# Kernel tuning notes

Hardware: AMD Instinct MI355X
Metric: run time of the kernel (lower is better)

## Reference

```python
import jax, jax.numpy as jnp
import numpy as np

H = 2048          # hidden_size
NH = 16           # num_attention_heads
NKV = 4           # num_key_value_heads
HD = 128          # head_dim
B, S = 2, 2048
EPS = 1e-6


def _rms_norm(x, w):
    # RMSNorm over last dim (head_dim)
    var = jnp.mean(jnp.square(x), axis=-1, keepdims=True)
    return x * jax.lax.rsqrt(var + EPS) * w


def _rotate_half(x):
    x1, x2 = jnp.split(x, 2, axis=-1)
    return jnp.concatenate([-x2, x1], axis=-1)


def _apply_rope(x, cos, sin):
    # x: [b, s, h, d]; cos/sin: [s, d]
    c = cos[None, :, None, :]
    s = sin[None, :, None, :]
    return x * c + _rotate_half(x) * s


def setup_inputs() -> dict:
    key = jax.random.key(0)
    ks = jax.random.split(key, 12)
    hidden_states = jax.random.normal(ks[0], (B, S, H), dtype=jnp.float32)
    # RoPE tables (base 10000, full head_dim)
    inv_freq = 1.0 / (10000.0 ** (np.arange(0, HD, 2, dtype=np.float32) / HD))
    t = np.arange(S, dtype=np.float32)
    freqs = np.outer(t, inv_freq)                      # [S, HD/2]
    emb = np.concatenate([freqs, freqs], axis=-1)      # [S, HD]
    cos = jnp.asarray(np.cos(emb), dtype=jnp.float32)
    sin = jnp.asarray(np.sin(emb), dtype=jnp.float32)
    scale = 0.02
    Wq = jax.random.normal(ks[1], (H, NH * HD), jnp.float32) * scale
    bq = jax.random.normal(ks[2], (NH * HD,), jnp.float32) * scale
    Wk = jax.random.normal(ks[3], (H, NKV * HD), jnp.float32) * scale
    bk = jax.random.normal(ks[4], (NKV * HD,), jnp.float32) * scale
    Wv = jax.random.normal(ks[5], (H, NKV * HD), jnp.float32) * scale
    bv = jax.random.normal(ks[6], (NKV * HD,), jnp.float32) * scale
    Wo = jax.random.normal(ks[7], (NH * HD, H), jnp.float32) * scale
    bo = jax.random.normal(ks[8], (H,), jnp.float32) * scale
    q_norm_w = jnp.ones((HD,), jnp.float32)
    k_norm_w = jnp.ones((HD,), jnp.float32)
    cu_seqlens = jnp.array([0, S, 2 * S], dtype=jnp.int32)
    max_s = S
    return {"hidden_states": hidden_states, "cos": cos, "sin": sin,
            "Wq": Wq, "bq": bq, "Wk": Wk, "bk": bk, "Wv": Wv, "bv": bv,
            "Wo": Wo, "bo": bo, "q_norm_w": q_norm_w, "k_norm_w": k_norm_w,
            "cu_seqlens": cu_seqlens, "max_s": max_s}


def reference(hidden_states, cos, sin, Wq, bq, Wk, bk, Wv, bv, Wo, bo,
              q_norm_w, k_norm_w, cu_seqlens, max_s):
    b, s, _ = hidden_states.shape
    q = (hidden_states @ Wq + bq).reshape(b, s, NH, HD)
    k = (hidden_states @ Wk + bk).reshape(b, s, NKV, HD)
    v = (hidden_states @ Wv + bv).reshape(b, s, NKV, HD)
    q = _rms_norm(q, q_norm_w)
    k = _rms_norm(k, k_norm_w)
    q = _apply_rope(q, cos, sin)
    k = _apply_rope(k, cos, sin)
    # GQA: repeat_interleave kv heads to match query heads
    n_rep = NH // NKV
    k = jnp.repeat(k, n_rep, axis=2)   # [b, s, NH, HD]
    v = jnp.repeat(v, n_rep, axis=2)
    scale = 1.0 / jnp.sqrt(jnp.float32(HD))
    # scores: [b, h, s_q, s_k]
    scores = jnp.einsum('bqhd,bkhd->bhqk', q, k) * scale
    neg = jnp.finfo(scores.dtype).min
    causal = jnp.triu(jnp.ones((s, s), dtype=bool), k=1)
    scores = scores + jnp.where(causal, neg, 0.0)[None, None]
    weights = jax.nn.softmax(scores, axis=-1)
    attn = jnp.einsum('bhqk,bkhd->bqhd', weights, v).reshape(b, s, NH * HD)
    return attn @ Wo + bo
```

## Files before the change

### kernel.cpp

```cpp
#include <hip/hip_runtime.h>
#include <math.h>

#define H 2048
#define NH 16
#define NKV 4
#define HD 128
#define BB 2
#define SS 2048
#define NT (BB*SS)
#define NQK (NH*HD)
#define NKVD (NKV*HD)
#define NQKV (NQK + 2*NKVD)
#define EPSV 1e-6f
#define SM_SCALE 0.08838834764831845f

using s8v = __attribute__((ext_vector_type(8))) short;
using s4v = __attribute__((ext_vector_type(4))) short;
using f4v = __attribute__((ext_vector_type(4))) float;

typedef unsigned int __attribute__((address_space(1))) u32_g;
typedef unsigned int __attribute__((address_space(3))) u32_l;

__device__ inline float bf2f(short s){ unsigned u = ((unsigned)(unsigned short)s) << 16; return __builtin_bit_cast(float, u); }
__device__ inline short f2bf(float f){ unsigned u = __builtin_bit_cast(unsigned, f); u += 0x7FFF + ((u>>16)&1); return (short)(u>>16); }

__device__ inline f4v mfma16(s8v a, s8v b, f4v c){
    return __builtin_amdgcn_mfma_f32_16x16x32_bf16(a, b, c, 0, 0, 0);
}

__device__ inline void gl_lds16(const short* g, short* l){
    __builtin_amdgcn_global_load_lds((const u32_g*)g, (u32_l*)l, 16, 0, 0);
}


__global__ void cvt_f32_bf16(const float* __restrict__ in, short* __restrict__ out, int n4){
    int i = blockIdx.x*blockDim.x + threadIdx.x;
    int stride = gridDim.x*blockDim.x;
    for (; i < n4; i += stride){
        float4 v = reinterpret_cast<const float4*>(in)[i];
        s4v o = { f2bf(v.x), f2bf(v.y), f2bf(v.z), f2bf(v.w) };
        reinterpret_cast<s4v*>(out)[i] = o;
    }
}

__global__ __launch_bounds__(256) void transpose_cvt(const float* __restrict__ src, short* __restrict__ dst,
                                                     int R, int C){
    __shared__ short t[64][72];
    const int tid = threadIdx.x;
    const int r0 = blockIdx.y*64, c0 = blockIdx.x*64;
    #pragma unroll
    for (int it = 0; it < 4; ++it){
        int ch = tid + it*256;
        int row = ch >> 4, c4 = (ch & 15) * 4;
        float4 v = *reinterpret_cast<const float4*>(src + (size_t)(r0+row)*C + c0 + c4);
        t[row][c4+0] = f2bf(v.x); t[row][c4+1] = f2bf(v.y);
        t[row][c4+2] = f2bf(v.z); t[row][c4+3] = f2bf(v.w);
    }
    __syncthreads();
    #pragma unroll
    for (int it = 0; it < 4; ++it){
        int ch = tid + it*256;
        int cc = ch >> 4, r4 = (ch & 15) * 4;
        s4v o = { t[r4+0][cc], t[r4+1][cc], t[r4+2][cc], t[r4+3][cc] };
        *reinterpret_cast<s4v*>(dst + (size_t)(c0+cc)*R + r0 + r4) = o;
    }
}

__global__ void concat_b(const float* __restrict__ bq, const float* __restrict__ bk,
                         const float* __restrict__ bv, float* __restrict__ Bc){
    int i = blockIdx.x*blockDim.x + threadIdx.x;
    if (i < NQKV)
        Bc[i] = (i < NQK) ? bq[i] : (i < NQK+NKVD ? bk[i-NQK] : bv[i-NQK-NKVD]);
}


template<int OUT_F32>
__global__ __launch_bounds__(256) void gemm_bt(const short* __restrict__ A, const short* __restrict__ BT,
                                               const float* __restrict__ bias, void* __restrict__ Cout,
                                               int M, int N, int K){
    __shared__ short As[2][4096];
    __shared__ short Bs[2][4096];
    const int tid  = threadIdx.x;
    const int lane = tid & 63;
    const int wv   = tid >> 6;
    const int f    = lane & 15;
    const int g    = lane >> 4;
    const int m0   = blockIdx.y * 128;
    const int n0   = blockIdx.x * 128;
    const int mb   = (wv & 1) * 64;
    const int nb   = (wv >> 1) * 64;
    f4v acc[4][4] = {};

    const short* Abase = A  + (size_t)m0*K;
    const short* Bbase = BT + (size_t)n0*K;
    const int srow = (lane >> 2);
    const int scol = (lane & 3) * 8;

    auto STAGE = [&](int buf, int k0){
        #pragma unroll
        for (int c = 0; c < 2; ++c){
            int issue = wv + c*4;
            int row = issue*16 + srow;
            gl_lds16(Abase + (size_t)row*K + k0 + scol, &As[buf][issue*512]);
            gl_lds16(Bbase + (size_t)row*K + k0 + scol, &Bs[buf][issue*512]);
        }
    };

    STAGE(0, 0);
    asm volatile("s_waitcnt vmcnt(0)" ::: "memory");
    __syncthreads();
    int cur = 0;
    for (int k0 = 0; k0 < K; k0 += 32){
        if (k0 + 32 < K) STAGE(cur^1, k0 + 32);
        s8v a[4], bfr[4];
        #pragma unroll
        for (int i = 0; i < 4; ++i) a[i]   = *reinterpret_cast<const s8v*>(&As[cur][(mb + i*16 + f)*32 + g*8]);
        #pragma unroll
        for (int j = 0; j < 4; ++j) bfr[j] = *reinterpret_cast<const s8v*>(&Bs[cur][(nb + j*16 + f)*32 + g*8]);
        #pragma unroll
        for (int i = 0; i < 4; ++i)
            #pragma unroll
            for (int j = 0; j < 4; ++j)
                acc[i][j] = mfma16(a[i], bfr[j], acc[i][j]);
        asm volatile("s_waitcnt vmcnt(0)" ::: "memory");
        __syncthreads();
        cur ^= 1;
    }

    #pragma unroll
    for (int i = 0; i < 4; ++i){
        #pragma unroll
        for (int j = 0; j < 4; ++j){
            int col = n0 + nb + j*16 + f;
            float bvv = bias ? bias[col] : 0.f;
            #pragma unroll
            for (int r = 0; r < 4; ++r){
                int row = m0 + mb + i*16 + g*4 + r;
                float vv = acc[i][j][r] + bvv;
                if (OUT_F32) reinterpret_cast<float*>(Cout)[(size_t)row*N + col] = vv;
                else         reinterpret_cast<short*>(Cout)[(size_t)row*N + col] = f2bf(vv);
            }
        }
    }
}


__global__ __launch_bounds__(256) void norm_rope(short* __restrict__ qkv, const float* __restrict__ cosb,
                                                 const float* __restrict__ sinb, const float* __restrict__ qw,
                                                 const float* __restrict__ kw){
    int row  = blockIdx.x * 4 + (threadIdx.x >> 6);
    int lane = threadIdx.x & 63;
    const int QROWS = NT * NH;
    short* ptr; const float* w; float outscale; int token;
    if (row < QROWS){
        token = row >> 4; int h = row & 15;
        ptr = qkv + (size_t)token*NQKV + h*HD; w = qw; outscale = SM_SCALE;
    } else {
        int rr = row - QROWS;
        token = rr >> 2; int h = rr & 3;
        ptr = qkv + (size_t)token*NQKV + NQK + h*HD; w = kw; outscale = 1.f;
    }
    int s = token & (SS-1);
    float x1 = bf2f(ptr[lane]), x2 = bf2f(ptr[lane+64]);
    float ssq = x1*x1 + x2*x2;
    #pragma unroll
    for (int off = 32; off; off >>= 1) ssq += __shfl_xor(ssq, off, 64);
    float inv = rsqrtf(ssq * (1.f/128.f) + EPSV);
    float n1 = x1 * inv * w[lane];
    float n2 = x2 * inv * w[lane+64];
    float c1 = cosb[s*HD + lane], c2 = cosb[s*HD + lane + 64];
    float s1 = sinb[s*HD + lane], s2 = sinb[s*HD + lane + 64];
    float o1 = (n1*c1 - n2*s1) * outscale;
    float o2 = (n2*c2 + n1*s2) * outscale;
    ptr[lane]    = f2bf(o1);
    ptr[lane+64] = f2bf(o2);
}


__global__ __launch_bounds__(256) void vtrans(const short* __restrict__ qkv, short* __restrict__ Vt){
    __shared__ short t[64][72];
    const int tid = threadIdx.x;
    const int s0 = blockIdx.x*64, c0 = blockIdx.y*64, b = blockIdx.z;
    #pragma unroll
    for (int it = 0; it < 2; ++it){
        int ch = tid + it*256;
        int row = ch >> 3, col = (ch & 7)*8;
        s8v v = *reinterpret_cast<const s8v*>(qkv + (size_t)(b*SS + s0 + row)*NQKV + NQK + NKVD + c0 + col);
        *reinterpret_cast<s8v*>(&t[row][col]) = v;
    }
    __syncthreads();
    #pragma unroll
    for (int it = 0; it < 2; ++it){
        int ch = tid + it*256;
        int cc = ch >> 3, sc = (ch & 7)*8;
        s8v o;
        #pragma unroll
        for (int j = 0; j < 8; ++j) o[j] = t[sc + j][cc];
        *reinterpret_cast<s8v*>(Vt + (size_t)(b*NKVD + c0 + cc)*SS + s0 + sc) = o;
    }
}


__global__ __launch_bounds__(512, 4) void attn_fwd(const short* __restrict__ qkv, const short* __restrict__ Vt,
                                                   short* __restrict__ attn){
    __shared__ short Ks[2][8192];
    __shared__ short Vs[2][8192];
    __shared__ short Ps[8][1024];
    const int tid  = threadIdx.x;
    const int lane = tid & 63;
    const int w    = tid >> 6;
    const int f    = lane & 15;
    const int g    = lane >> 4;
    const int qt   = 63 - (int)blockIdx.x;
    const int kvh  = blockIdx.y;
    const int b    = blockIdx.z;
    const int h    = kvh*4 + (w >> 1);
    const int half = w & 1;
    const int q0   = qt * 32;
    const int qrow0 = q0 + half*16;
    char* Pb = (char*)Ps[w];

    auto STAGEK = [&](int buf, int kv0){
        #pragma unroll
        for (int c = 0; c < 2; ++c){
            int issue = w + c*8;
            int row = issue*4 + g;
            int col16 = f ^ (row & 7);
            gl_lds16(qkv + (size_t)(b*SS + kv0 + row)*NQKV + NQK + kvh*HD + col16*8,
                     &Ks[buf][issue*512]);
        }
    };
    auto STAGEV = [&](int buf, int kv0){
        #pragma unroll
        for (int c = 0; c < 2; ++c){
            int issue = w + c*8;
            int row = issue*8 + (lane >> 3);
            int col16 = (lane & 7) ^ (row & 7);
            gl_lds16(Vt + (size_t)(b*NKVD + kvh*HD + row)*SS + kv0 + col16*8,
                     &Vs[buf][issue*512]);
        }
    };

    s8v qa[4];
    #pragma unroll
    for (int dc = 0; dc < 4; ++dc)
        qa[dc] = *reinterpret_cast<const s8v*>(
            qkv + (size_t)(b*SS + qrow0 + f)*NQKV + h*HD + dc*32 + g*8);

    f4v acc[8] = {};
    float m_[4], l_[4];
    #pragma unroll
    for (int r = 0; r < 4; ++r){ m_[r] = -3e38f; l_[r] = 0.f; }

    const int nt = (q0 + 32 + 63) >> 6;
    STAGEK(0, 0);
    STAGEV(0, 0);
    asm volatile("s_waitcnt vmcnt(0)" ::: "memory");
    __builtin_amdgcn_sched_barrier(0);
    __builtin_amdgcn_s_barrier();
    int cur = 0;

    for (int t = 0; t < nt; ++t){
        const int kv0 = t*64;
        if (t + 1 < nt){ STAGEK(cur^1, kv0 + 64); STAGEV(cur^1, kv0 + 64); }

        f4v sf[4] = {};
        #pragma unroll
        for (int kh = 0; kh < 4; ++kh){
            const int krow = kh*16 + f;
            #pragma unroll
            for (int dc = 0; dc < 4; ++dc){
                s8v kb = *reinterpret_cast<const s8v*>(
                    (const char*)Ks[cur] + krow*256 + ((dc*64 + g*16) ^ ((krow & 7) << 4)));
                sf[kh] = mfma16(qa[dc], kb, sf[kh]);
            }
        }

        if (kv0 + 63 > qrow0){
            #pragma unroll
            for (int kh = 0; kh < 4; ++kh){
                int key = kv0 + kh*16 + f;
                #pragma unroll
                for (int r = 0; r < 4; ++r){
                    int qrow = qrow0 + g*4 + r;
                    if (key > qrow) sf[kh][r] = -3e38f;
                }
            }
        }

        float pm[4];
        bool need = false;
        #pragma unroll
        for (int r = 0; r < 4; ++r){
            float mx = fmaxf(fmaxf(sf[0][r], sf[1][r]), fmaxf(sf[2][r], sf[3][r]));
            #pragma unroll
            for (int off = 8; off; off >>= 1) mx = fmaxf(mx, __shfl_xor(mx, off, 16));
            pm[r] = mx;
            need = need || (mx > m_[r] + 8.f);
        }
        if (__any(need)){
            #pragma unroll
            for (int r = 0; r < 4; ++r){
                float mn = fmaxf(m_[r], pm[r]);
                float al = __expf(m_[r] - mn);
                m_[r] = mn;
                l_[r] *= al;
                #pragma unroll
                for (int df = 0; df < 8; ++df) acc[df][r] *= al;
            }
        }

        #pragma unroll
        for (int r = 0; r < 4; ++r){
            const int prow = g*4 + r;
            float ps = 0.f;
            #pragma unroll
            for (int kh = 0; kh < 4; ++kh){
                float p = __expf(sf[kh][r] - m_[r]);
                short pb = f2bf(p);
                ps += bf2f(pb);
                *(short*)(Pb + prow*128 + ((unsigned)((kh*16 + f)*2) ^ ((prow & 7) << 4))) = pb;
            }
            #pragma unroll
            for (int off = 8; off; off >>= 1) ps += __shfl_xor(ps, off, 16);
            l_[r] += ps;
        }

        #pragma unroll
        for (int ks = 0; ks < 2; ++ks){
            s8v pa = *reinterpret_cast<const s8v*>(
                Pb + f*128 + ((ks*64 + g*16) ^ ((f & 7) << 4)));
            #pragma unroll
            for (int df = 0; df < 8; ++df){
                const int vrow = df*16 + f;
                s8v vb = *reinterpret_cast<const s8v*>(
                    (const char*)Vs[cur] + vrow*128 + ((ks*64 + g*16) ^ ((vrow & 7) << 4)));
                acc[df] = mfma16(pa, vb, acc[df]);
            }
        }

        asm volatile("s_waitcnt vmcnt(0)" ::: "memory");
        __builtin_amdgcn_sched_barrier(0);
        __builtin_amdgcn_s_barrier();
        cur ^= 1;
    }

    #pragma unroll
    for (int r = 0; r < 4; ++r){
        int qrow = qrow0 + g*4 + r;
        float inv = 1.f / l_[r];
        short* ob = attn + (size_t)(b*SS + qrow)*NQK + h*HD;
        #pragma unroll
        for (int df = 0; df < 8; ++df)
            ob[df*16 + f] = f2bf(acc[df][r] * inv);
    }
}


extern "C" void kernel_launch(void* const* d_in, const int* in_sizes, int n_in,
                              void* d_out, int out_size, void* d_ws, size_t ws_size,
                              hipStream_t stream){
    (void)in_sizes; (void)n_in; (void)out_size; (void)ws_size;
    const float* hs   = (const float*)d_in[0];
    const float* cosb = (const float*)d_in[1];
    const float* sinb = (const float*)d_in[2];
    const float* Wq   = (const float*)d_in[3];
    const float* bq   = (const float*)d_in[4];
    const float* Wk   = (const float*)d_in[5];
    const float* bk   = (const float*)d_in[6];
    const float* Wv   = (const float*)d_in[7];
    const float* bv   = (const float*)d_in[8];
    const float* Wo   = (const float*)d_in[9];
    const float* bo   = (const float*)d_in[10];
    const float* qw   = (const float*)d_in[11];
    const float* kw   = (const float*)d_in[12];
    float* out = (float*)d_out;
    char* ws = (char*)d_ws;

    size_t off = 0;
    auto alloc = [&](size_t bytes){ size_t o = off; off += (bytes + 255) & ~(size_t)255; return o; };
    short* Xb    = (short*)(ws + alloc((size_t)NT*H*2));
    short* Wct   = (short*)(ws + alloc((size_t)NQKV*H*2));
    float* Bc    = (float*)(ws + alloc((size_t)NQKV*4));
    short* QKV   = (short*)(ws + alloc((size_t)NT*NQKV*2));
    short* Vt    = (short*)(ws + alloc((size_t)BB*NKVD*SS*2 + 4096));
    short* attnb = (short*)(ws + alloc((size_t)NT*NQK*2));
    short* WoT   = (short*)(ws + alloc((size_t)H*NQK*2));

    cvt_f32_bf16<<<2048, 256, 0, stream>>>(hs, Xb, NT*H/4);
    transpose_cvt<<<dim3(NQK/64,  H/64), 256, 0, stream>>>(Wq, Wct,                        H, NQK);
    transpose_cvt<<<dim3(NKVD/64, H/64), 256, 0, stream>>>(Wk, Wct + (size_t)NQK*H,        H, NKVD);
    transpose_cvt<<<dim3(NKVD/64, H/64), 256, 0, stream>>>(Wv, Wct + (size_t)(NQK+NKVD)*H, H, NKVD);
    transpose_cvt<<<dim3(H/64,  NQK/64), 256, 0, stream>>>(Wo, WoT,                        NQK, H);
    concat_b<<<3, 1024, 0, stream>>>(bq, bk, bv, Bc);

    gemm_bt<0><<<dim3(NQKV/128, NT/128), 256, 0, stream>>>(Xb, Wct, Bc, QKV, NT, NQKV, H);
    norm_rope<<<(NT*(NH+NKV))/4, 256, 0, stream>>>(QKV, cosb, sinb, qw, kw);
    vtrans<<<dim3(SS/64, NKVD/64, BB), 256, 0, stream>>>(QKV, Vt);
    attn_fwd<<<dim3(64, NKV, BB), 512, 0, stream>>>(QKV, Vt, attnb);
    gemm_bt<1><<<dim3(H/128, NT/128), 256, 0, stream>>>(attnb, WoT, bo, out, NT, H, NQK);
}
```

Baseline: 411.5 us.

## Streamline attention softmax with exp2, deferred row sums, priority hints and block swizzles

The log2(e) factor is folded into the query scale in norm_rope, so attention can use the hardware exp2 directly. The per-tile row-sum shuffle reduction becomes a per-lane partial sum, reduced once in the epilogue. The row-max shuffle now runs only when a rescale is actually needed, with the lazy-rescale threshold set to 11 in log2 units. It also adds s_setprio around the MFMA loops, flattens the attention grid so each query tile's 8 (head, batch) blocks launch together, and adds an XCD-aware block swizzle to the GEMMs for better L2 locality. Together these cut VALU/shuffle work per tile, at the cost of somewhat larger unnormalized intermediate values.

Measured after the change: 349.8 us. 15.0% less time.

```diff
diff --git a/kernel.cpp b/kernel.cpp
--- a/kernel.cpp
+++ b/kernel.cpp
@@ -13,6 +13,7 @@
 #define NQKV (NQK + 2*NKVD)
 #define EPSV 1e-6f
 #define SM_SCALE 0.08838834764831845f
+#define LOG2E 1.4426950408889634f
 
 using s8v = __attribute__((ext_vector_type(8))) short;
 using s4v = __attribute__((ext_vector_type(4))) short;
@@ -85,8 +86,13 @@
     const int wv   = tid >> 6;
     const int f    = lane & 15;
     const int g    = lane >> 4;
-    const int m0   = blockIdx.y * 128;
-    const int n0   = blockIdx.x * 128;
+
+    int lin = blockIdx.y * gridDim.x + blockIdx.x;
+    int cpx = (gridDim.x * gridDim.y) >> 3;
+    int sw  = (lin & 7) * cpx + (lin >> 3);
+    const int m0 = (sw / gridDim.x) * 128;
+    const int n0 = (sw % gridDim.x) * 128;
+
     const int mb   = (wv & 1) * 64;
     const int nb   = (wv >> 1) * 64;
     f4v acc[4][4] = {};
@@ -154,7 +160,7 @@
     short* ptr; const float* w; float outscale; int token;
     if (row < QROWS){
         token = row >> 4; int h = row & 15;
-        ptr = qkv + (size_t)token*NQKV + h*HD; w = qw; outscale = SM_SCALE;
+        ptr = qkv + (size_t)token*NQKV + h*HD; w = qw; outscale = SM_SCALE * LOG2E;
     } else {
         int rr = row - QROWS;
         token = rr >> 2; int h = rr & 3;
@@ -211,9 +217,10 @@
     const int w    = tid >> 6;
     const int f    = lane & 15;
     const int g    = lane >> 4;
-    const int qt   = 63 - (int)blockIdx.x;
-    const int kvh  = blockIdx.y;
-    const int b    = blockIdx.z;
+    const int bx   = blockIdx.x;
+    const int qt   = 63 - (bx >> 3);
+    const int kvh  = bx & 3;
+    const int b    = (bx >> 2) & 1;
     const int h    = kvh*4 + (w >> 1);
     const int half = w & 1;
     const int q0   = qt * 32;
@@ -248,9 +255,9 @@
             qkv + (size_t)(b*SS + qrow0 + f)*NQKV + h*HD + dc*32 + g*8);
 
     f4v acc[8] = {};
-    float m_[4], l_[4];
-    #pragma unroll
-    for (int r = 0; r < 4; ++r){ m_[r] = -3e38f; l_[r] = 0.f; }
+    float m_[4], lp_[4];
+    #pragma unroll
+    for (int r = 0; r < 4; ++r){ m_[r] = -3e38f; lp_[r] = 0.f; }
 
     const int nt = (q0 + 32 + 63) >> 6;
     STAGEK(0, 0);
@@ -265,6 +272,7 @@
         if (t + 1 < nt){ STAGEK(cur^1, kv0 + 64); STAGEV(cur^1, kv0 + 64); }
 
         f4v sf[4] = {};
+        __builtin_amdgcn_s_setprio(1);
         #pragma unroll
         for (int kh = 0; kh < 4; ++kh){
             const int krow = kh*16 + f;
@@ -275,6 +283,7 @@
                 sf[kh] = mfma16(qa[dc], kb, sf[kh]);
             }
         }
+        __builtin_amdgcn_s_setprio(0);
 
         if (kv0 + 63 > qrow0){
             #pragma unroll
@@ -288,23 +297,23 @@
             }
         }
 
-        float pm[4];
+        float mloc[4];
         bool need = false;
         #pragma unroll
         for (int r = 0; r < 4; ++r){
-            float mx = fmaxf(fmaxf(sf[0][r], sf[1][r]), fmaxf(sf[2][r], sf[3][r]));
-            #pragma unroll
-            for (int off = 8; off; off >>= 1) mx = fmaxf(mx, __shfl_xor(mx, off, 16));
-            pm[r] = mx;
-            need = need || (mx > m_[r] + 8.f);
+            mloc[r] = fmaxf(fmaxf(sf[0][r], sf[1][r]), fmaxf(sf[2][r], sf[3][r]));
+            need = need || (mloc[r] > m_[r] + 11.0f);
         }
         if (__any(need)){
             #pragma unroll
             for (int r = 0; r < 4; ++r){
-                float mn = fmaxf(m_[r], pm[r]);
-                float al = __expf(m_[r] - mn);
+                float mx = mloc[r];
+                #pragma unroll
+                for (int off = 8; off; off >>= 1) mx = fmaxf(mx, __shfl_xor(mx, off, 16));
+                float mn = fmaxf(m_[r], mx);
+                float al = __builtin_amdgcn_exp2f(m_[r] - mn);
                 m_[r] = mn;
-                l_[r] *= al;
+                lp_[r] *= al;
                 #pragma unroll
                 for (int df = 0; df < 8; ++df) acc[df][r] *= al;
             }
@@ -313,19 +322,16 @@
         #pragma unroll
         for (int r = 0; r < 4; ++r){
             const int prow = g*4 + r;
-            float ps = 0.f;
             #pragma unroll
             for (int kh = 0; kh < 4; ++kh){
-                float p = __expf(sf[kh][r] - m_[r]);
+                float p = __builtin_amdgcn_exp2f(sf[kh][r] - m_[r]);
                 short pb = f2bf(p);
-                ps += bf2f(pb);
+                lp_[r] += bf2f(pb);
                 *(short*)(Pb + prow*128 + ((unsigned)((kh*16 + f)*2) ^ ((prow & 7) << 4))) = pb;
             }
-            #pragma unroll
-            for (int off = 8; off; off >>= 1) ps += __shfl_xor(ps, off, 16);
-            l_[r] += ps;
-        }
-
+        }
+
+        __builtin_amdgcn_s_setprio(1);
         #pragma unroll
         for (int ks = 0; ks < 2; ++ks){
             s8v pa = *reinterpret_cast<const s8v*>(
@@ -338,6 +344,7 @@
                 acc[df] = mfma16(pa, vb, acc[df]);
             }
         }
+        __builtin_amdgcn_s_setprio(0);
 
         asm volatile("s_waitcnt vmcnt(0)" ::: "memory");
         __builtin_amdgcn_sched_barrier(0);
@@ -347,8 +354,11 @@
 
     #pragma unroll
     for (int r = 0; r < 4; ++r){
+        float l = lp_[r];
+        #pragma unroll
+        for (int off = 8; off; off >>= 1) l += __shfl_xor(l, off, 16);
         int qrow = qrow0 + g*4 + r;
-        float inv = 1.f / l_[r];
+        float inv = 1.f / l;
         short* ob = attn + (size_t)(b*SS + qrow)*NQK + h*HD;
         #pragma unroll
         for (int df = 0; df < 8; ++df)
@@ -397,6 +407,6 @@
     gemm_bt<0><<<dim3(NQKV/128, NT/128), 256, 0, stream>>>(Xb, Wct, Bc, QKV, NT, NQKV, H);
     norm_rope<<<(NT*(NH+NKV))/4, 256, 0, stream>>>(QKV, cosb, sinb, qw, kw);
     vtrans<<<dim3(SS/64, NKVD/64, BB), 256, 0, stream>>>(QKV, Vt);
-    attn_fwd<<<dim3(64, NKV, BB), 512, 0, stream>>>(QKV, Vt, attnb);
+    attn_fwd<<<512, 512, 0, stream>>>(QKV, Vt, attnb);
     gemm_bt<1><<<dim3(H/128, NT/128), 256, 0, stream>>>(attnb, WoT, bo, out, NT, H, NQK);
 }
```
